# Optimization experiments

Measured on AMD Instinct MI355X. Metric: run time of the kernel, lower is better.

Reference implementation:

```python
import jax, jax.numpy as jnp
import numpy as np

NEG_SLOPE = 0.1  # LReLu_neg_slope
WEIGHT_INIT_STD = 1.0
N_GEN, N_LOAD, N_END = 25000, 25000, 25000
N_NODES = 100000
N_EDGES = 1600000
H = 128
N_HIDDEN_LAYERS = 3  # N_GCN_layers - 1


def _lin_w(key, n_in, n_out):
    # torch init: normal(std = weight_init_std / in_channels); stored as (in, out) for jax
    return jax.random.normal(key, (n_in, n_out), dtype=jnp.float32) * (WEIGHT_INIT_STD / n_in)


def setup_inputs() -> dict:
    key = jax.random.key(0)
    ks = jax.random.split(key, 24)
    inp = {
        "x_gen": jax.random.normal(ks[0], (N_GEN, 3), dtype=jnp.float32),
        "x_load": jax.random.normal(ks[1], (N_LOAD, 3), dtype=jnp.float32),
        "x_or": jax.random.normal(ks[2], (N_END, 6), dtype=jnp.float32),
        "x_ex": jax.random.normal(ks[3], (N_END, 6), dtype=jnp.float32),
        "edge_index": jax.random.randint(ks[4], (2, N_EDGES), 0, N_NODES, dtype=jnp.int64)
        if jax.config.jax_enable_x64 else jax.random.randint(ks[4], (2, N_EDGES), 0, N_NODES, dtype=jnp.int32),
        "object_ptv": jnp.arange(N_NODES, dtype=jnp.int32),
    }
    # per-type embedding MLPs (2 Linear layers each)
    inp["Wg1"], inp["bg1"] = _lin_w(ks[5], 3, H), jnp.zeros((H,), jnp.float32)
    inp["Wg2"], inp["bg2"] = _lin_w(ks[6], H, H), jnp.zeros((H,), jnp.float32)
    inp["Wld1"], inp["bld1"] = _lin_w(ks[7], 3, H), jnp.zeros((H,), jnp.float32)
    inp["Wld2"], inp["bld2"] = _lin_w(ks[8], H, H), jnp.zeros((H,), jnp.float32)
    inp["Wor1"], inp["bor1"] = _lin_w(ks[9], 6, H), jnp.zeros((H,), jnp.float32)
    inp["Wor2"], inp["bor2"] = _lin_w(ks[10], H, H), jnp.zeros((H,), jnp.float32)
    inp["Wex1"], inp["bex1"] = _lin_w(ks[11], 6, H), jnp.zeros((H,), jnp.float32)
    inp["Wex2"], inp["bex2"] = _lin_w(ks[12], H, H), jnp.zeros((H,), jnp.float32)
    # hidden SAGEConv layers (stacked): lin_l (neighbor, with bias) + lin_r (root, no bias)
    inp["Wl_h"] = jnp.stack([_lin_w(ks[13 + i], H, H) for i in range(N_HIDDEN_LAYERS)])
    inp["bl_h"] = jnp.zeros((N_HIDDEN_LAYERS, H), jnp.float32)
    inp["Wr_h"] = jnp.stack([_lin_w(ks[16 + i], H, H) for i in range(N_HIDDEN_LAYERS)])
    # output SAGEConv layer -> 1 unit
    inp["Wl_o"], inp["bl_o"] = _lin_w(ks[19], H, 1), jnp.zeros((1,), jnp.float32)
    inp["Wr_o"] = _lin_w(ks[20], H, 1)
    return inp


def _lrelu(x):
    return jax.nn.leaky_relu(x, NEG_SLOPE)


def _embed(x, W1, b1, W2, b2):
    return _lrelu(_lrelu(x @ W1 + b1) @ W2 + b2)


def reference(x_gen, x_load, x_or, x_ex, edge_index, object_ptv,
              Wg1, bg1, Wg2, bg2, Wld1, bld1, Wld2, bld2,
              Wor1, bor1, Wor2, bor2, Wex1, bex1, Wex2, bex2,
              Wl_h, bl_h, Wr_h, Wl_o, bl_o, Wr_o):
    x = jnp.concatenate([
        _embed(x_gen, Wg1, bg1, Wg2, bg2),
        _embed(x_load, Wld1, bld1, Wld2, bld2),
        _embed(x_or, Wor1, bor1, Wor2, bor2),
        _embed(x_ex, Wex1, bex1, Wex2, bex2),
    ], axis=0)
    x = x[object_ptv]                      # [N, H] in topology-vector order
    src, dst = edge_index[0], edge_index[1]
    n = x.shape[0]
    deg = jax.ops.segment_sum(jnp.ones_like(src, dtype=x.dtype), dst, num_segments=n)
    inv_deg = (1.0 / jnp.maximum(deg, 1.0))[:, None]

    def sage(h, Wl, bl, Wr):
        # SAGEConv(aggr='mean', root_weight=True): lin_l(mean_j h_j) + bias + lin_r(h_i)
        agg = jax.ops.segment_sum(h[src], dst, num_segments=n) * inv_deg
        return agg @ Wl + bl + h @ Wr

    for i in range(Wl_h.shape[0]):
        x = _lrelu(sage(x, Wl_h[i], bl_h[i], Wr_h[i]))
    return jax.nn.sigmoid(sage(x, Wl_o, bl_o, Wr_o))  # [N, 1]
```

## Files before the change

kernel.cpp:

```cpp
#include <hip/hip_runtime.h>
#include <hip/hip_bf16.h>
#include <math.h>

#define HD 128
#define NPB 512
#define CAP 16384
#define SCHUNK 4096
#define ALCSR 768

typedef __attribute__((ext_vector_type(8))) short  bf16x8;
typedef __attribute__((ext_vector_type(4))) float  f32x4;

__device__ __forceinline__ float lrelu(float v) { return v > 0.0f ? v : 0.1f * v; }

__device__ __forceinline__ unsigned short f2bf(float f) {
  union { float f; unsigned u; } c; c.f = f;
  unsigned u = c.u + 0x7fffu + ((c.u >> 16) & 1u);
  return (unsigned short)(u >> 16);
}
__device__ __forceinline__ float bf2f(unsigned short u) {
  return __uint_as_float((unsigned)u << 16);
}

__global__ __launch_bounds__(256)
void embed1_kernel(const float* __restrict__ xg, const float* __restrict__ xl,
                   const float* __restrict__ xo, const float* __restrict__ xe,
                   const float* __restrict__ Wg, const float* __restrict__ bg,
                   const float* __restrict__ Wl, const float* __restrict__ bl,
                   const float* __restrict__ Wo, const float* __restrict__ bo,
                   const float* __restrict__ We, const float* __restrict__ be,
                   unsigned short* __restrict__ h1, int4 padCum, int4 realCnt) {
  int p = blockIdx.x * 2 + (threadIdx.x >> 7);
  if (p >= padCum.w) return;
  int j = threadIdx.x & 127;
  int typ = (p < padCum.x) ? 0 : (p < padCum.y) ? 1 : (p < padCum.z) ? 2 : 3;
  int padStart = (typ == 0) ? 0 : (typ == 1) ? padCum.x : (typ == 2) ? padCum.y : padCum.z;
  int cnt = (typ == 0) ? realCnt.x : (typ == 1) ? realCnt.y : (typ == 2) ? realCnt.z : realCnt.w;
  int loc = p - padStart;
  if (loc >= cnt) return;
  const float *x, *W, *bb; int IN;
  if (typ == 0)      { x = xg; W = Wg; bb = bg; IN = 3; }
  else if (typ == 1) { x = xl; W = Wl; bb = bl; IN = 3; }
  else if (typ == 2) { x = xo; W = Wo; bb = bo; IN = 6; }
  else               { x = xe; W = We; bb = be; IN = 6; }
  float acc = bb[j];
  for (int k = 0; k < IN; k++) acc += x[(size_t)loc * IN + k] * W[k * HD + j];
  h1[(size_t)p * HD + j] = f2bf(lrelu(acc));
}

__global__ __launch_bounds__(256)
void wprep_all_kernel(const float* __restrict__ Wg2, const float* __restrict__ Wld2,
                      const float* __restrict__ Wor2, const float* __restrict__ Wex2,
                      const float* __restrict__ Wl_h, const float* __restrict__ Wr_h,
                      unsigned short* __restrict__ Wp,
                      const int* __restrict__ ptv, int* __restrict__ inv,
                      int* __restrict__ gcnt, int n) {
  int tid = blockIdx.x * 256 + threadIdx.x;
  if (tid < 256) gcnt[tid] = 0;
  if (tid < n) inv[ptv[tid]] = tid;
  int m = tid >> 14;
  int i = tid & 16383;
  const float* src; unsigned short* dst;
  switch (m) {
    case 0: src = Wg2;  dst = Wp;             break;
    case 1: src = Wld2; dst = Wp + 16384;     break;
    case 2: src = Wor2; dst = Wp + 2 * 16384; break;
    case 3: src = Wex2; dst = Wp + 3 * 16384; break;
    default: {
      int mm = m - 4; int l = mm >> 1; int isR = mm & 1;
      src = (isR ? Wr_h : Wl_h) + (size_t)l * 16384;
      dst = Wp + 4 * 16384 + (size_t)l * 32768 + (isR ? 16384 : 0);
    }
  }
  int k = i >> 7, j = i & 127;
  int ks = k >> 5, g = (k >> 3) & 3, b = k & 7;
  dst[((ks * 128 + j) * 4 + g) * 8 + b] = f2bf(src[i]);
}

__global__ __launch_bounds__(256)
void mfma_embed2_kernel(const unsigned short* __restrict__ h1,
                        const unsigned short* __restrict__ Wp,
                        const float* __restrict__ b_g, const float* __restrict__ b_ld,
                        const float* __restrict__ b_or, const float* __restrict__ b_ex,
                        const int* __restrict__ inv, unsigned short* __restrict__ out,
                        int4 padCum, int4 realStart, int4 realCnt) {
  const int t = threadIdx.x, w = t >> 6, l = t & 63;
  const int lr = l & 15, lg = l >> 4;
  const int prow0 = blockIdx.x * 64 + w * 16;
  int typ = (prow0 < padCum.x) ? 0 : (prow0 < padCum.y) ? 1 : (prow0 < padCum.z) ? 2 : 3;
  int padStart = (typ == 0) ? 0 : (typ == 1) ? padCum.x : (typ == 2) ? padCum.y : padCum.z;
  int rStart = (typ == 0) ? realStart.x : (typ == 1) ? realStart.y : (typ == 2) ? realStart.z : realStart.w;
  int cnt = (typ == 0) ? realCnt.x : (typ == 1) ? realCnt.y : (typ == 2) ? realCnt.z : realCnt.w;
  const float* bias = (typ == 0) ? b_g : (typ == 1) ? b_ld : (typ == 2) ? b_or : b_ex;

  int raLoc = prow0 + lr - padStart; if (raLoc >= cnt) raLoc = cnt - 1;
  const unsigned short* abase = h1 + (size_t)(padStart + raLoc) * HD + 8 * lg;
  const unsigned short* wbase = Wp + (size_t)typ * 16384 + lr * 32 + lg * 8;

  f32x4 acc[8];
  #pragma unroll
  for (int cb = 0; cb < 8; cb++) {
    float bv = bias[cb * 16 + lr];
    acc[cb] = (f32x4){bv, bv, bv, bv};
  }
  #pragma unroll
  for (int ks = 0; ks < 4; ks++) {
    bf16x8 af = *(const bf16x8*)(abase + ks * 32);
    #pragma unroll
    for (int cb = 0; cb < 8; cb++) {
      bf16x8 bfv = *(const bf16x8*)(wbase + (size_t)(ks * 128 + cb * 16) * 32);
      acc[cb] = __builtin_amdgcn_mfma_f32_16x16x32_bf16(af, bfv, acc[cb], 0, 0, 0);
    }
  }
  int tgt[4];
  #pragma unroll
  for (int r = 0; r < 4; r++) {
    int locRow = prow0 + lg * 4 + r - padStart;
    tgt[r] = (locRow < cnt) ? inv[rStart + locRow] : -1;
  }
  #pragma unroll
  for (int cb = 0; cb < 8; cb++) {
    #pragma unroll
    for (int r = 0; r < 4; r++) {
      if (tgt[r] >= 0)
        out[(size_t)tgt[r] * HD + cb * 16 + lr] = f2bf(lrelu(acc[cb][r]));
    }
  }
}

__global__ __launch_bounds__(256)
void bucket_scatter_kernel(const int* __restrict__ esrc, const int* __restrict__ edst,
                           int* __restrict__ gcnt, int* __restrict__ ebuf, int nE) {
  __shared__ int cnt[256];
  __shared__ int cur[256];
  const int t = threadIdx.x;
  const int c0 = blockIdx.x * SCHUNK;
  int s_arr[16], d_arr[16];
  cnt[t] = 0;
  __syncthreads();
  #pragma unroll
  for (int k = 0; k < 16; k++) {
    int idx = c0 + k * 256 + t;
    if (idx < nE) {
      s_arr[k] = esrc[idx];
      int d = edst[idx];
      d_arr[k] = d;
      atomicAdd(&cnt[d >> 9], 1);
    } else d_arr[k] = -1;
  }
  __syncthreads();
  if (cnt[t] > 0) cur[t] = atomicAdd(&gcnt[t], cnt[t]);
  __syncthreads();
  #pragma unroll
  for (int k = 0; k < 16; k++) {
    if (d_arr[k] >= 0) {
      int b = d_arr[k] >> 9;
      int p = atomicAdd(&cur[b], 1);
      ebuf[(size_t)b * CAP + p] = (s_arr[k] << 9) | (d_arr[k] & 511);
    }
  }
}

__device__ __forceinline__ int wave_incl_scan(int v) {
  int lane = threadIdx.x & 63;
  #pragma unroll
  for (int d = 1; d < 64; d <<= 1) {
    int tv = __shfl_up(v, d, 64);
    if (lane >= d) v += tv;
  }
  return v;
}

__global__ __launch_bounds__(256)
void bucket_build_kernel(const int* __restrict__ ebuf, const int* __restrict__ gcnt,
                         int* __restrict__ csr, int* __restrict__ offs,
                         int* __restrict__ deg, float* __restrict__ inv_deg, int n) {
  __shared__ int hist[512];
  __shared__ int offl[512];
  __shared__ int wsum[4];
  const int b = blockIdx.x, t = threadIdx.x;
  const int cnt = gcnt[b];
  const size_t ebase = (size_t)b * CAP;
  hist[t] = 0; hist[t + 256] = 0;
  __syncthreads();
  for (int i = t; i < cnt; i += 256) {
    int e = ebuf[ebase + i];
    atomicAdd(&hist[e & 511], 1);
  }
  __syncthreads();
  int a0 = hist[2 * t], a1 = hist[2 * t + 1];
  int s = a0 + a1;
  int incl = wave_incl_scan(s);
  int wid = t >> 6;
  if ((t & 63) == 63) wsum[wid] = incl;
  __syncthreads();
  int wbase = 0;
  for (int w_ = 0; w_ < wid; w_++) wbase += wsum[w_];
  int excl = wbase + incl - s;
  offl[2 * t] = excl;
  offl[2 * t + 1] = excl + a0;
  __syncthreads();
  const int d0 = b << 9;
  for (int i = t; i < 512; i += 256) {
    int g = d0 + i;
    if (g < n) {
      offs[g] = b * CAP + offl[i];
      int dg = hist[i];
      deg[g] = dg;
      inv_deg[g] = 1.0f / fmaxf((float)dg, 1.0f);
    }
  }
  __syncthreads();
  for (int i = t; i < cnt; i += 256) {
    int e = ebuf[ebase + i];
    int p = atomicAdd(&offl[e & 511], 1);
    csr[ebase + p] = ((unsigned)e) >> 9;
  }
}

template<bool EMIT_Z>
__global__ __launch_bounds__(256)
void sage_fused_kernel(const unsigned short* __restrict__ x, const int* __restrict__ csr,
                       const int* __restrict__ offs, const int* __restrict__ deg,
                       const float* __restrict__ inv_deg,
                       const unsigned short* __restrict__ Wp, const float* __restrict__ bias,
                       unsigned short* __restrict__ out,
                       const float* __restrict__ wl, const float* __restrict__ wr,
                       float* __restrict__ zl, float* __restrict__ zr, int n) {
  __shared__ int lcsr[ALCSR];
  __shared__ __align__(16) unsigned short lagg[16][136];
  __shared__ float zpart[2][4][16];
  const int t = threadIdx.x;
  const int node0 = blockIdx.x * 16;
  int last = node0 + 15; if (last >= n) last = n - 1;
  const int s_begin = offs[node0];
  const int total = offs[last] + deg[last] - s_begin;
  const bool useLds = (total <= ALCSR);
  if (useLds) {
    for (int k = t; k < total; k += 256) lcsr[k] = csr[s_begin + k];
  }
  __syncthreads();

  const int w = t >> 6, l = t & 63;
  {
    const int g = l >> 4, j = l & 15;
    const int node = node0 + w * 4 + g;
    if (node < n) {
      const unsigned short* xj = x + 8 * j;
      const int lb = offs[node] - s_begin;
      const int d = deg[node];
      float2 a0[4] = {{0.f,0.f},{0.f,0.f},{0.f,0.f},{0.f,0.f}};
      float2 a1[4] = {{0.f,0.f},{0.f,0.f},{0.f,0.f},{0.f,0.f}};
      int i = 0;
      if (useLds) {
        for (; i + 1 < d; i += 2) {
          int e0 = lcsr[lb + i], e1 = lcsr[lb + i + 1];
          uint4 v0 = *(const uint4*)(xj + (size_t)e0 * HD);
          uint4 v1 = *(const uint4*)(xj + (size_t)e1 * HD);
          const unsigned w0[4] = {v0.x, v0.y, v0.z, v0.w};
          const unsigned w1[4] = {v1.x, v1.y, v1.z, v1.w};
          #pragma unroll
          for (int k = 0; k < 4; k++) {
            a0[k] = make_float2(a0[k].x + __uint_as_float(w0[k] << 16),
                                a0[k].y + __uint_as_float(w0[k] & 0xffff0000u));
            a1[k] = make_float2(a1[k].x + __uint_as_float(w1[k] << 16),
                                a1[k].y + __uint_as_float(w1[k] & 0xffff0000u));
          }
        }
        if (i < d) {
          int e0 = lcsr[lb + i];
          uint4 v0 = *(const uint4*)(xj + (size_t)e0 * HD);
          const unsigned w0[4] = {v0.x, v0.y, v0.z, v0.w};
          #pragma unroll
          for (int k = 0; k < 4; k++)
            a0[k] = make_float2(a0[k].x + __uint_as_float(w0[k] << 16),
                                a0[k].y + __uint_as_float(w0[k] & 0xffff0000u));
        }
      } else {
        const int* gcsr = csr + s_begin + lb;
        for (; i + 1 < d; i += 2) {
          int e0 = gcsr[i], e1 = gcsr[i + 1];
          uint4 v0 = *(const uint4*)(xj + (size_t)e0 * HD);
          uint4 v1 = *(const uint4*)(xj + (size_t)e1 * HD);
          const unsigned w0[4] = {v0.x, v0.y, v0.z, v0.w};
          const unsigned w1[4] = {v1.x, v1.y, v1.z, v1.w};
          #pragma unroll
          for (int k = 0; k < 4; k++) {
            a0[k] = make_float2(a0[k].x + __uint_as_float(w0[k] << 16),
                                a0[k].y + __uint_as_float(w0[k] & 0xffff0000u));
            a1[k] = make_float2(a1[k].x + __uint_as_float(w1[k] << 16),
                                a1[k].y + __uint_as_float(w1[k] & 0xffff0000u));
          }
        }
        if (i < d) {
          int e0 = gcsr[i];
          uint4 v0 = *(const uint4*)(xj + (size_t)e0 * HD);
          const unsigned w0[4] = {v0.x, v0.y, v0.z, v0.w};
          #pragma unroll
          for (int k = 0; k < 4; k++)
            a0[k] = make_float2(a0[k].x + __uint_as_float(w0[k] << 16),
                                a0[k].y + __uint_as_float(w0[k] & 0xffff0000u));
        }
      }
      const float id = inv_deg[node];
      uint4 o;
      unsigned* op = (unsigned*)&o;
      #pragma unroll
      for (int k = 0; k < 4; k++) {
        float lo = (a0[k].x + a1[k].x) * id;
        float hi = (a0[k].y + a1[k].y) * id;
        op[k] = (unsigned)f2bf(lo) | ((unsigned)f2bf(hi) << 16);
      }
      *(uint4*)&lagg[w * 4 + g][j * 8] = o;
    }
  }
  __syncthreads();

  const int lr = l & 15, lg = l >> 4;
  int ra = node0 + lr; if (ra >= n) ra = n - 1;
  const unsigned short* wbase = Wp + (size_t)lr * 32 + (size_t)lg * 8;
  const unsigned short* rbase = x + (size_t)ra * HD + 8 * lg;

  f32x4 acc[2];
  #pragma unroll
  for (int c = 0; c < 2; c++) {
    float bv = bias[(2 * w + c) * 16 + lr];
    acc[c] = (f32x4){bv, bv, bv, bv};
  }
  #pragma unroll
  for (int ks = 0; ks < 4; ks++) {
    bf16x8 af = *(const bf16x8*)&lagg[lr][lg * 8 + ks * 32];
    #pragma unroll
    for (int c = 0; c < 2; c++) {
      int cb = 2 * w + c;
      bf16x8 bfv = *(const bf16x8*)(wbase + (size_t)(ks * 128 + cb * 16) * 32);
      acc[c] = __builtin_amdgcn_mfma_f32_16x16x32_bf16(af, bfv, acc[c], 0, 0, 0);
    }
  }
  #pragma unroll
  for (int ks = 0; ks < 4; ks++) {
    bf16x8 af = *(const bf16x8*)(rbase + ks * 32);
    #pragma unroll
    for (int c = 0; c < 2; c++) {
      int cb = 2 * w + c;
      bf16x8 bfv = *(const bf16x8*)(wbase + (size_t)((4 + ks) * 128 + cb * 16) * 32);
      acc[c] = __builtin_amdgcn_mfma_f32_16x16x32_bf16(af, bfv, acc[c], 0, 0, 0);
    }
  }

  if constexpr (!EMIT_Z) {
    #pragma unroll
    for (int c = 0; c < 2; c++) {
      int cb = 2 * w + c;
      #pragma unroll
      for (int r = 0; r < 4; r++) {
        int node = node0 + lg * 4 + r;
        if (node < n)
          out[(size_t)node * HD + cb * 16 + lr] = f2bf(lrelu(acc[c][r]));
      }
    }
  } else {
    float vl[4] = {0.f, 0.f, 0.f, 0.f}, vr[4] = {0.f, 0.f, 0.f, 0.f};
    #pragma unroll
    for (int c = 0; c < 2; c++) {
      int cb = 2 * w + c;
      float wlv = wl[cb * 16 + lr];
      float wrv = wr[cb * 16 + lr];
      #pragma unroll
      for (int r = 0; r < 4; r++) {
        float x3 = lrelu(acc[c][r]);
        vl[r] += x3 * wlv;
        vr[r] += x3 * wrv;
      }
    }
    #pragma unroll
    for (int r = 0; r < 4; r++) {
      #pragma unroll
      for (int d = 1; d < 16; d <<= 1) {
        vl[r] += __shfl_xor(vl[r], d, 64);
        vr[r] += __shfl_xor(vr[r], d, 64);
      }
    }
    if (lr == 0) {
      #pragma unroll
      for (int r = 0; r < 4; r++) {
        zpart[0][w][lg * 4 + r] = vl[r];
        zpart[1][w][lg * 4 + r] = vr[r];
      }
    }
    __syncthreads();
    if (t < 16) {
      int node = node0 + t;
      if (node < n) {
        zl[node] = zpart[0][0][t] + zpart[0][1][t] + zpart[0][2][t] + zpart[0][3][t];
        zr[node] = zpart[1][0][t] + zpart[1][1][t] + zpart[1][2][t] + zpart[1][3][t];
      }
    }
  }
}

__global__ __launch_bounds__(256)
void zfinal_kernel(const float* __restrict__ zl, const float* __restrict__ zr,
                   const int* __restrict__ csr, const int* __restrict__ offs,
                   const int* __restrict__ deg, const float* __restrict__ inv_deg,
                   const float* __restrict__ bl, float* __restrict__ out, int n) {
  int i = blockIdx.x * 256 + threadIdx.x;
  if (i >= n) return;
  int s0 = offs[i], d = deg[i];
  float a = 0.f;
  #pragma unroll 4
  for (int e = 0; e < d; e++) a += zl[csr[s0 + e]];
  float s = a * inv_deg[i] + bl[0] + zr[i];
  out[i] = 1.0f / (1.0f + expf(-s));
}

extern "C" void kernel_launch(void* const* d_in, const int* in_sizes, int n_in,
                              void* d_out, int out_size, void* d_ws, size_t ws_size,
                              hipStream_t stream) {
  const float* x_gen  = (const float*)d_in[0];
  const float* x_load = (const float*)d_in[1];
  const float* x_or   = (const float*)d_in[2];
  const float* x_ex   = (const float*)d_in[3];
  const int*   edge   = (const int*)d_in[4];
  const int*   ptv    = (const int*)d_in[5];
  const float* Wg1  = (const float*)d_in[6],  *bg1  = (const float*)d_in[7];
  const float* Wg2  = (const float*)d_in[8],  *bg2  = (const float*)d_in[9];
  const float* Wld1 = (const float*)d_in[10], *bld1 = (const float*)d_in[11];
  const float* Wld2 = (const float*)d_in[12], *bld2 = (const float*)d_in[13];
  const float* Wor1 = (const float*)d_in[14], *bor1 = (const float*)d_in[15];
  const float* Wor2 = (const float*)d_in[16], *bor2 = (const float*)d_in[17];
  const float* Wex1 = (const float*)d_in[18], *bex1 = (const float*)d_in[19];
  const float* Wex2 = (const float*)d_in[20], *bex2 = (const float*)d_in[21];
  const float* Wl_h = (const float*)d_in[22], *bl_h = (const float*)d_in[23];
  const float* Wr_h = (const float*)d_in[24];
  const float* Wl_o = (const float*)d_in[25], *bl_o = (const float*)d_in[26];
  const float* Wr_o = (const float*)d_in[27];

  const int n_gen  = in_sizes[0] / 3;
  const int n_load = in_sizes[1] / 3;
  const int n_or   = in_sizes[2] / 6;
  const int n_ex   = in_sizes[3] / 6;
  const int nE     = in_sizes[4] / 2;
  const int N      = in_sizes[5];
  const int* esrc = edge;
  const int* edst = edge + nE;

  const int np0 = ((n_gen  + 63) / 64) * 64;
  const int np1 = ((n_load + 63) / 64) * 64;
  const int np2 = ((n_or   + 63) / 64) * 64;
  const int np3 = ((n_ex   + 63) / 64) * 64;
  const int NP  = np0 + np1 + np2 + np3;
  const int4 padCum    = make_int4(np0, np0 + np1, np0 + np1 + np2, NP);
  const int4 realStart = make_int4(0, n_gen, n_gen + n_load, n_gen + n_load + n_or);
  const int4 realCnt   = make_int4(n_gen, n_load, n_or, n_ex);

  const int NB = (N + NPB - 1) / NPB;

  size_t NPel = (size_t)NP * HD;
  size_t nel  = (size_t)N * HD;
  unsigned short* b0 = (unsigned short*)d_ws;
  unsigned short* b1 = b0 + NPel;
  unsigned short* b3 = b1 + nel;
  int*  gcnt = (int*)(b3 + nel);
  int*  ebuf = gcnt + 256;
  int*  csr  = ebuf + (size_t)NB * CAP;
  int*  offs = csr + (size_t)NB * CAP;
  int*  deg  = offs + N;
  float* inv_deg = (float*)(deg + N);
  float* zl = inv_deg + N;
  float* zr = zl + N;
  int*  invp = (int*)(zr + N);
  uintptr_t wp_addr = ((uintptr_t)(invp + N) + 15) & ~(uintptr_t)15;
  unsigned short* Wp = (unsigned short*)wp_addr;

  wprep_all_kernel<<<640, 256, 0, stream>>>(Wg2, Wld2, Wor2, Wex2, Wl_h, Wr_h, Wp,
                                            ptv, invp, gcnt, N);

  embed1_kernel<<<NP / 2, 256, 0, stream>>>(x_gen, x_load, x_or, x_ex,
                                            Wg1, bg1, Wld1, bld1, Wor1, bor1, Wex1, bex1,
                                            b0, padCum, realCnt);
  mfma_embed2_kernel<<<NP / 64, 256, 0, stream>>>(b0, Wp, bg2, bld2, bor2, bex2,
                                                  invp, b1, padCum, realStart, realCnt);

  bucket_scatter_kernel<<<(nE + SCHUNK - 1) / SCHUNK, 256, 0, stream>>>(esrc, edst, gcnt, ebuf, nE);
  bucket_build_kernel<<<NB, 256, 0, stream>>>(ebuf, gcnt, csr, offs, deg, inv_deg, N);

  const int fGrid = (N + 15) / 16;
  const unsigned short* WpC = Wp + 4 * 16384;
  unsigned short* xcur = b1;
  unsigned short* xnext = b3;
  for (int l = 0; l < 2; l++) {
    sage_fused_kernel<false><<<fGrid, 256, 0, stream>>>(
        xcur, csr, offs, deg, inv_deg, WpC + (size_t)l * 32768,
        bl_h + (size_t)l * HD, xnext, nullptr, nullptr, nullptr, nullptr, N);
    unsigned short* tmp = xcur; xcur = xnext; xnext = tmp;
  }
  sage_fused_kernel<true><<<fGrid, 256, 0, stream>>>(
      xcur, csr, offs, deg, inv_deg, WpC + 2 * 32768,
      bl_h + 2 * HD, nullptr, Wl_o, Wr_o, zl, zr, N);

  zfinal_kernel<<<(N + 255) / 256, 256, 0, stream>>>(zl, zr, csr, offs, deg, inv_deg,
                                                     bl_o, (float*)d_out, N);
}
```

Baseline: 345.2 us.

## Process 32 nodes per block in fused SAGE kernel with 4-way gather unroll

The fused SAGE kernel now handles 32 nodes per block instead of 16. Each wave gathers two groups of nodes, and the neighbor gather is unrolled four ways with four independent accumulators to expose more memory-level parallelism. The MFMA phase computes two 16-row tiles per wave, reusing each loaded weight fragment twice and halving weight traffic per node. Costs are higher register pressure, a larger LDS CSR staging buffer, and half as many blocks, which may reduce occupancy or load balance.

```diff
diff --git a/kernel.cpp b/kernel.cpp
--- a/kernel.cpp
+++ b/kernel.cpp
@@ -6,7 +6,8 @@
 #define NPB 512
 #define CAP 16384
 #define SCHUNK 4096
-#define ALCSR 768
+#define FTILE 32
+#define ALCSR 1536
 
 typedef __attribute__((ext_vector_type(8))) short  bf16x8;
 typedef __attribute__((ext_vector_type(4))) float  f32x4;
@@ -228,11 +229,11 @@
                        const float* __restrict__ wl, const float* __restrict__ wr,
                        float* __restrict__ zl, float* __restrict__ zr, int n) {
   __shared__ int lcsr[ALCSR];
-  __shared__ __align__(16) unsigned short lagg[16][136];
-  __shared__ float zpart[2][4][16];
+  __shared__ __align__(16) unsigned short lagg[FTILE][136];
+  __shared__ float zpart[2][4][FTILE];
   const int t = threadIdx.x;
-  const int node0 = blockIdx.x * 16;
-  int last = node0 + 15; if (last >= n) last = n - 1;
+  const int node0 = blockIdx.x * FTILE;
+  int last = node0 + FTILE - 1; if (last >= n) last = n - 1;
   const int s_begin = offs[node0];
   const int total = offs[last] + deg[last] - s_begin;
   const bool useLds = (total <= ALCSR);
@@ -244,152 +245,160 @@
   const int w = t >> 6, l = t & 63;
   {
     const int g = l >> 4, j = l & 15;
-    const int node = node0 + w * 4 + g;
-    if (node < n) {
-      const unsigned short* xj = x + 8 * j;
-      const int lb = offs[node] - s_begin;
-      const int d = deg[node];
-      float2 a0[4] = {{0.f,0.f},{0.f,0.f},{0.f,0.f},{0.f,0.f}};
-      float2 a1[4] = {{0.f,0.f},{0.f,0.f},{0.f,0.f},{0.f,0.f}};
-      int i = 0;
-      if (useLds) {
-        for (; i + 1 < d; i += 2) {
-          int e0 = lcsr[lb + i], e1 = lcsr[lb + i + 1];
-          uint4 v0 = *(const uint4*)(xj + (size_t)e0 * HD);
-          uint4 v1 = *(const uint4*)(xj + (size_t)e1 * HD);
-          const unsigned w0[4] = {v0.x, v0.y, v0.z, v0.w};
-          const unsigned w1[4] = {v1.x, v1.y, v1.z, v1.w};
+    const unsigned short* xj = x + 8 * j;
+    #pragma unroll
+    for (int p = 0; p < 2; p++) {
+      const int nrow = w * 8 + p * 4 + g;
+      const int node = node0 + nrow;
+      if (node < n) {
+        const int lb = offs[node] - s_begin;
+        const int d = deg[node];
+        float ac[4][8];
+        #pragma unroll
+        for (int c = 0; c < 4; c++)
           #pragma unroll
-          for (int k = 0; k < 4; k++) {
-            a0[k] = make_float2(a0[k].x + __uint_as_float(w0[k] << 16),
-                                a0[k].y + __uint_as_float(w0[k] & 0xffff0000u));
-            a1[k] = make_float2(a1[k].x + __uint_as_float(w1[k] << 16),
-                                a1[k].y + __uint_as_float(w1[k] & 0xffff0000u));
+          for (int q = 0; q < 8; q++) ac[c][q] = 0.f;
+
+        auto accum = [&](int c, uint4 v) {
+          const unsigned q0 = v.x, q1 = v.y, q2 = v.z, q3 = v.w;
+          ac[c][0] += __uint_as_float(q0 << 16); ac[c][1] += __uint_as_float(q0 & 0xffff0000u);
+          ac[c][2] += __uint_as_float(q1 << 16); ac[c][3] += __uint_as_float(q1 & 0xffff0000u);
+          ac[c][4] += __uint_as_float(q2 << 16); ac[c][5] += __uint_as_float(q2 & 0xffff0000u);
+          ac[c][6] += __uint_as_float(q3 << 16); ac[c][7] += __uint_as_float(q3 & 0xffff0000u);
+        };
+        int i = 0;
+        if (useLds) {
+          const int* eb = lcsr + lb;
+          for (; i + 3 < d; i += 4) {
+            uint4 v0 = *(const uint4*)(xj + (size_t)eb[i]     * HD);
+            uint4 v1 = *(const uint4*)(xj + (size_t)eb[i + 1] * HD);
+            uint4 v2 = *(const uint4*)(xj + (size_t)eb[i + 2] * HD);
+            uint4 v3 = *(const uint4*)(xj + (size_t)eb[i + 3] * HD);
+            accum(0, v0); accum(1, v1); accum(2, v2); accum(3, v3);
           }
+          for (; i < d; i++) accum(i & 3, *(const uint4*)(xj + (size_t)eb[i] * HD));
+        } else {
+          const int* eb = csr + s_begin + lb;
+          for (; i + 3 < d; i += 4) {
+            uint4 v0 = *(const uint4*)(xj + (size_t)eb[i]     * HD);
+            uint4 v1 = *(const uint4*)(xj + (size_t)eb[i + 1] * HD);
+            uint4 v2 = *(const uint4*)(xj + (size_t)eb[i + 2] * HD);
+            uint4 v3 = *(const uint4*)(xj + (size_t)eb[i + 3] * HD);
+            accum(0, v0); accum(1, v1); accum(2, v2); accum(3, v3);
+          }
+          for (; i < d; i++) accum(i & 3, *(const uint4*)(xj + (size_t)eb[i] * HD));
         }
-        if (i < d) {
-          int e0 = lcsr[lb + i];
-          uint4 v0 = *(const uint4*)(xj + (size_t)e0 * HD);
-          const unsigned w0[4] = {v0.x, v0.y, v0.z, v0.w};
-          #pragma unroll
-          for (int k = 0; k < 4; k++)
-            a0[k] = make_float2(a0[k].x + __uint_as_float(w0[k] << 16),
-                                a0[k].y + __uint_as_float(w0[k] & 0xffff0000u));
+        const float id = inv_deg[node];
+        uint4 o;
+        unsigned* op = (unsigned*)&o;
+        #pragma unroll
+        for (int k = 0; k < 4; k++) {
+          float lo = (ac[0][2*k]   + ac[1][2*k]   + ac[2][2*k]   + ac[3][2*k])   * id;
+          float hi = (ac[0][2*k+1] + ac[1][2*k+1] + ac[2][2*k+1] + ac[3][2*k+1]) * id;
+          op[k] = (unsigned)f2bf(lo) | ((unsigned)f2bf(hi) << 16);
         }
+        *(uint4*)&lagg[nrow][j * 8] = o;
       } else {
-        const int* gcsr = csr + s_begin + lb;
-        for (; i + 1 < d; i += 2) {
-          int e0 = gcsr[i], e1 = gcsr[i + 1];
-          uint4 v0 = *(const uint4*)(xj + (size_t)e0 * HD);
-          uint4 v1 = *(const uint4*)(xj + (size_t)e1 * HD);
-          const unsigned w0[4] = {v0.x, v0.y, v0.z, v0.w};
-          const unsigned w1[4] = {v1.x, v1.y, v1.z, v1.w};
-          #pragma unroll
-          for (int k = 0; k < 4; k++) {
-            a0[k] = make_float2(a0[k].x + __uint_as_float(w0[k] << 16),
-                                a0[k].y + __uint_as_float(w0[k] & 0xffff0000u));
-            a1[k] = make_float2(a1[k].x + __uint_as_float(w1[k] << 16),
-                                a1[k].y + __uint_as_float(w1[k] & 0xffff0000u));
-          }
-        }
-        if (i < d) {
-          int e0 = gcsr[i];
-          uint4 v0 = *(const uint4*)(xj + (size_t)e0 * HD);
-          const unsigned w0[4] = {v0.x, v0.y, v0.z, v0.w};
-          #pragma unroll
-          for (int k = 0; k < 4; k++)
-            a0[k] = make_float2(a0[k].x + __uint_as_float(w0[k] << 16),
-                                a0[k].y + __uint_as_float(w0[k] & 0xffff0000u));
-        }
+        *(uint4*)&lagg[nrow][j * 8] = make_uint4(0, 0, 0, 0);
       }
-      const float id = inv_deg[node];
-      uint4 o;
-      unsigned* op = (unsigned*)&o;
-      #pragma unroll
-      for (int k = 0; k < 4; k++) {
-        float lo = (a0[k].x + a1[k].x) * id;
-        float hi = (a0[k].y + a1[k].y) * id;
-        op[k] = (unsigned)f2bf(lo) | ((unsigned)f2bf(hi) << 16);
-      }
-      *(uint4*)&lagg[w * 4 + g][j * 8] = o;
     }
   }
   __syncthreads();
 
   const int lr = l & 15, lg = l >> 4;
-  int ra = node0 + lr; if (ra >= n) ra = n - 1;
+  int ra0 = node0 + lr;      if (ra0 >= n) ra0 = n - 1;
+  int ra1 = node0 + 16 + lr; if (ra1 >= n) ra1 = n - 1;
   const unsigned short* wbase = Wp + (size_t)lr * 32 + (size_t)lg * 8;
-  const unsigned short* rbase = x + (size_t)ra * HD + 8 * lg;
-
-  f32x4 acc[2];
+  const unsigned short* rbase0 = x + (size_t)ra0 * HD + 8 * lg;
+  const unsigned short* rbase1 = x + (size_t)ra1 * HD + 8 * lg;
+
+  f32x4 acc[2][2];
   #pragma unroll
   for (int c = 0; c < 2; c++) {
     float bv = bias[(2 * w + c) * 16 + lr];
-    acc[c] = (f32x4){bv, bv, bv, bv};
+    acc[0][c] = (f32x4){bv, bv, bv, bv};
+    acc[1][c] = (f32x4){bv, bv, bv, bv};
   }
   #pragma unroll
   for (int ks = 0; ks < 4; ks++) {
-    bf16x8 af = *(const bf16x8*)&lagg[lr][lg * 8 + ks * 32];
+    bf16x8 a0 = *(const bf16x8*)&lagg[lr][lg * 8 + ks * 32];
+    bf16x8 a1 = *(const bf16x8*)&lagg[16 + lr][lg * 8 + ks * 32];
     #pragma unroll
     for (int c = 0; c < 2; c++) {
       int cb = 2 * w + c;
       bf16x8 bfv = *(const bf16x8*)(wbase + (size_t)(ks * 128 + cb * 16) * 32);
-      acc[c] = __builtin_amdgcn_mfma_f32_16x16x32_bf16(af, bfv, acc[c], 0, 0, 0);
+      acc[0][c] = __builtin_amdgcn_mfma_f32_16x16x32_bf16(a0, bfv, acc[0][c], 0, 0, 0);
+      acc[1][c] = __builtin_amdgcn_mfma_f32_16x16x32_bf16(a1, bfv, acc[1][c], 0, 0, 0);
     }
   }
   #pragma unroll
   for (int ks = 0; ks < 4; ks++) {
-    bf16x8 af = *(const bf16x8*)(rbase + ks * 32);
+    bf16x8 a0 = *(const bf16x8*)(rbase0 + ks * 32);
+    bf16x8 a1 = *(const bf16x8*)(rbase1 + ks * 32);
     #pragma unroll
     for (int c = 0; c < 2; c++) {
       int cb = 2 * w + c;
       bf16x8 bfv = *(const bf16x8*)(wbase + (size_t)((4 + ks) * 128 + cb * 16) * 32);
-      acc[c] = __builtin_amdgcn_mfma_f32_16x16x32_bf16(af, bfv, acc[c], 0, 0, 0);
+      acc[0][c] = __builtin_amdgcn_mfma_f32_16x16x32_bf16(a0, bfv, acc[0][c], 0, 0, 0);
+      acc[1][c] = __builtin_amdgcn_mfma_f32_16x16x32_bf16(a1, bfv, acc[1][c], 0, 0, 0);
     }
   }
 
   if constexpr (!EMIT_Z) {
     #pragma unroll
-    for (int c = 0; c < 2; c++) {
-      int cb = 2 * w + c;
+    for (int rt = 0; rt < 2; rt++) {
       #pragma unroll
-      for (int r = 0; r < 4; r++) {
-        int node = node0 + lg * 4 + r;
-        if (node < n)
-          out[(size_t)node * HD + cb * 16 + lr] = f2bf(lrelu(acc[c][r]));
+      for (int c = 0; c < 2; c++) {
+        int cb = 2 * w + c;
+        #pragma unroll
+        for (int r = 0; r < 4; r++) {
+          int node = node0 + rt * 16 + lg * 4 + r;
+          if (node < n)
+            out[(size_t)node * HD + cb * 16 + lr] = f2bf(lrelu(acc[rt][c][r]));
+        }
       }
     }
   } else {
-    float vl[4] = {0.f, 0.f, 0.f, 0.f}, vr[4] = {0.f, 0.f, 0.f, 0.f};
+    float vl[2][4] = {{0.f,0.f,0.f,0.f},{0.f,0.f,0.f,0.f}};
+    float vr[2][4] = {{0.f,0.f,0.f,0.f},{0.f,0.f,0.f,0.f}};
     #pragma unroll
     for (int c = 0; c < 2; c++) {
       int cb = 2 * w + c;
       float wlv = wl[cb * 16 + lr];
       float wrv = wr[cb * 16 + lr];
       #pragma unroll
+      for (int rt = 0; rt < 2; rt++) {
+        #pragma unroll
+        for (int r = 0; r < 4; r++) {
+          float x3 = lrelu(acc[rt][c][r]);
+          vl[rt][r] += x3 * wlv;
+          vr[rt][r] += x3 * wrv;
+        }
+      }
+    }
+    #pragma unroll
+    for (int rt = 0; rt < 2; rt++) {
+      #pragma unroll
       for (int r = 0; r < 4; r++) {
-        float x3 = lrelu(acc[c][r]);
-        vl[r] += x3 * wlv;
-        vr[r] += x3 * wrv;
-      }
-    }
-    #pragma unroll
-    for (int r = 0; r < 4; r++) {
-      #pragma unroll
-      for (int d = 1; d < 16; d <<= 1) {
-        vl[r] += __shfl_xor(vl[r], d, 64);
-        vr[r] += __shfl_xor(vr[r], d, 64);
+        #pragma unroll
+        for (int d = 1; d < 16; d <<= 1) {
+          vl[rt][r] += __shfl_xor(vl[rt][r], d, 64);
+          vr[rt][r] += __shfl_xor(vr[rt][r], d, 64);
+        }
       }
     }
     if (lr == 0) {
       #pragma unroll
-      for (int r = 0; r < 4; r++) {
-        zpart[0][w][lg * 4 + r] = vl[r];
-        zpart[1][w][lg * 4 + r] = vr[r];
+      for (int rt = 0; rt < 2; rt++) {
+        #pragma unroll
+        for (int r = 0; r < 4; r++) {
+          zpart[0][w][rt * 16 + lg * 4 + r] = vl[rt][r];
+          zpart[1][w][rt * 16 + lg * 4 + r] = vr[rt][r];
+        }
       }
     }
     __syncthreads();
-    if (t < 16) {
+    if (t < FTILE) {
       int node = node0 + t;
       if (node < n) {
         zl[node] = zpart[0][0][t] + zpart[0][1][t] + zpart[0][2][t] + zpart[0][3][t];
@@ -485,7 +494,7 @@
   bucket_scatter_kernel<<<(nE + SCHUNK - 1) / SCHUNK, 256, 0, stream>>>(esrc, edst, gcnt, ebuf, nE);
   bucket_build_kernel<<<NB, 256, 0, stream>>>(ebuf, gcnt, csr, offs, deg, inv_deg, N);
 
-  const int fGrid = (N + 15) / 16;
+  const int fGrid = (N + FTILE - 1) / FTILE;
   const unsigned short* WpC = Wp + 4 * 16384;
   unsigned short* xcur = b1;
   unsigned short* xnext = b3;
```

Measured after the change: 717.6 us. 2.08x slower.
